# Kernel tuning notes

Measured on AMD Instinct MI355X. Metric: run time of the kernel, lower is better.

## Reference

```python
import jax, jax.numpy as jnp
import numpy as np

NEG_SLOPE = 0.2  # LeakyReLU slope used by standard DGCNN blocks


def _lrelu(v):
    return jnp.where(v >= 0, v, NEG_SLOPE * v)


def _knn_idx(pos, k):
    # pos: [B, N, 3] -> idx: [B, N, k] nearest neighbors by squared distance
    sq = jnp.sum(pos * pos, axis=-1)                       # [B, N]
    d2 = sq[:, :, None] - 2.0 * jnp.einsum('bnc,bmc->bnm', pos, pos) + sq[:, None, :]
    _, idx = jax.lax.top_k(-d2, k)                          # [B, N, k]
    return idx


def _edge_block(x, idx, wa, ba, wb, bb):
    # x: [B, N, C]; idx: [B, N, k]
    nb = jax.vmap(lambda xb, ib: xb[ib])(x, idx)            # [B, N, k, C] gather
    xc = jnp.broadcast_to(x[:, :, None, :], nb.shape)
    feat = jnp.concatenate([xc, nb - xc], axis=-1)          # 'local_global' edge feature [B,N,k,2C]
    h = _lrelu(jnp.einsum('bnkc,cd->bnkd', feat, wa) + ba)
    h = _lrelu(jnp.einsum('bnkc,cd->bnkd', h, wb) + bb)
    return jnp.max(h, axis=2)                               # maxpool over k neighbors -> [B, N, out]


def setup_inputs() -> dict:
    key = jax.random.key(0)
    ks = jax.random.split(key, 24)
    B, N, C = 8, 2048, 3

    def w(k, i, o):
        return jax.random.normal(k, (i, o), jnp.float32) * (1.0 / np.sqrt(i))

    inp = {
        'x': jax.random.normal(ks[0], (B, N, C), jnp.float32),
        'pos': jax.random.normal(ks[1], (B, N, 3), jnp.float32),
        # block1: 2*3 -> 64 -> 64
        'w1a': w(ks[2], 6, 64), 'b1a': jnp.zeros((64,), jnp.float32),
        'w1b': w(ks[3], 64, 64), 'b1b': jnp.zeros((64,), jnp.float32),
        # block2: 2*64 -> 64 -> 128
        'w2a': w(ks[4], 128, 64), 'b2a': jnp.zeros((64,), jnp.float32),
        'w2b': w(ks[5], 64, 128), 'b2b': jnp.zeros((128,), jnp.float32),
        # block3: 2*128 -> 128 -> 512
        'w3a': w(ks[6], 256, 128), 'b3a': jnp.zeros((128,), jnp.float32),
        'w3b': w(ks[7], 128, 512), 'b3b': jnp.zeros((512,), jnp.float32),
        # final head: 704 -> 512 -> 256 -> 12
        'wf1': w(ks[8], 704, 512), 'bf1': jnp.zeros((512,), jnp.float32),
        'wf2': w(ks[9], 512, 256), 'bf2': jnp.zeros((256,), jnp.float32),
        'wf3': w(ks[10], 256, 12), 'bf3': jnp.zeros((12,), jnp.float32),
    }
    return inp


def reference(x, pos, w1a, b1a, w1b, b1b, w2a, b2a, w2b, b2b, w3a, b3a, w3b, b3b,
              wf1, bf1, wf2, bf2, wf3, bf3):
    k = 32
    # kNN graph is built from pos in every block; pos is constant so idx is identical
    idx = _knn_idx(pos, k)
    x1 = _edge_block(x, idx, w1a, b1a, w1b, b1b)            # [B, N, 64]
    x2 = _edge_block(x1, idx, w2a, b2a, w2b, b2b)           # [B, N, 128]
    x3 = _edge_block(x2, idx, w3a, b3a, w3b, b3b)           # [B, N, 512]
    h = jnp.concatenate([x1, x2, x3], axis=2)               # [B, N, 704]
    h = _lrelu(h @ wf1 + bf1)
    h = _lrelu(h @ wf2 + bf2)
    return h @ wf3 + bf3                                    # [B, N, 12]
```

## Files before the change

### kernel.cpp

```cpp
#include <hip/hip_runtime.h>

typedef unsigned short u16;
typedef unsigned int u32;
typedef unsigned long long u64;
typedef short bf16x8 __attribute__((ext_vector_type(8)));
typedef float f32x4 __attribute__((ext_vector_type(4)));
typedef u32 u32x4 __attribute__((ext_vector_type(4)));

__device__ __forceinline__ float b2f(u16 u) {
    return __uint_as_float(((u32)u) << 16);
}
__device__ __forceinline__ u16 f2b(float f) {
    u32 u = __float_as_uint(f);
    u32 r = u + 0x7fffu + ((u >> 16) & 1u);
    return (u16)(r >> 16);
}
__device__ __forceinline__ f32x4 mfma16(bf16x8 a, bf16x8 b, f32x4 c) {
    return __builtin_amdgcn_mfma_f32_16x16x32_bf16(a, b, c, 0, 0, 0);
}

template<int NP, int KP, int R, int C>
__device__ __forceinline__ bool seg(int t, int base, const float* src, u16* dst) {
    int r = t - base;
    if (r < 0) return true;
    constexpr int RNG = NP * KP;
    if (r >= RNG) return false;
    int n = r / KP, k = r - n * KP;
    float v = (k < R && n < C) ? src[k * C + n] : 0.f;
    u16 hi = f2b(v);
    dst[r] = hi;
    dst[RNG + r] = f2b(v - b2f(hi));
    return true;
}
template<int NP, int KP, int R, int C>
__device__ __forceinline__ bool seg_bf(int t, int base, const float* src, u16* dst) {
    int r = t - base;
    if (r < 0) return true;
    constexpr int RNG = NP * KP;
    if (r >= RNG) return false;
    constexpr int KC = KP / 32;
    int j = r & 7, s = r >> 3;
    int lanei = s & 63;
    int ks = (s >> 6) % KC, tile = (s >> 6) / KC;
    int n = tile * 16 + (lanei & 15);
    int k = ks * 32 + (lanei >> 4) * 8 + j;
    float v = (k < R && n < C) ? src[k * C + n] : 0.f;
    u16 hi = f2b(v);
    dst[r] = hi;
    dst[RNG + r] = f2b(v - b2f(hi));
    return true;
}
template<int CMID, int CIN, int KP>
__device__ __forceinline__ bool seg_uv(int t, int base, const float* wa, u16* dst) {
    int r = t - base;
    if (r < 0) return true;
    constexpr int RNG = 2 * CMID * KP;
    if (r >= RNG) return false;
    int n = r / KP, k = r - n * KP;
    float v = 0.f;
    if (k < CIN) {
        if (n < CMID) v = wa[k * CMID + n] - wa[(CIN + k) * CMID + n];
        else          v = wa[(CIN + k) * CMID + (n - CMID)];
    }
    u16 hi = f2b(v);
    dst[r] = hi;
    dst[RNG + r] = f2b(v - b2f(hi));
    return true;
}

__global__ __launch_bounds__(256) void prep_weights(
    const float* w1a, const float* w1b, const float* w2a, const float* w2b,
    const float* w3a, const float* w3b, const float* wf1, const float* wf2,
    const float* wf3,
    u16* t1uv, u16* t2uv, u16* t3uv, u16* t1b, u16* t2b, u16* t3b,
    u16* tf1, u16* tf2, u16* tf3)
{
    int t = blockIdx.x * 256 + threadIdx.x;
    if (seg_uv< 64,   3,  32>(t,      0, w1a, t1uv)) return;
    if (seg_uv< 64,  64,  64>(t,   4096, w2a, t2uv)) return;
    if (seg_uv<128, 128, 128>(t,  12288, w3a, t3uv)) return;
    if (seg_bf< 64,  64,  64,  64>(t,  45056, w1b, t1b)) return;
    if (seg_bf<128,  64,  64, 128>(t,  49152, w2b, t2b)) return;
    if (seg_bf<512, 128, 128, 512>(t,  57344, w3b, t3b)) return;
    if (seg<512, 704, 704, 512>(t, 122880, wf1, tf1)) return;
    if (seg<256, 512, 512, 256>(t, 483328, wf2, tf2)) return;
    if (seg< 16, 256, 256,  12>(t, 614400, wf3, tf3)) return;
}

__device__ __forceinline__ void bitonic256(double v[4], int lane) {
#pragma unroll
    for (int k = 2; k <= 256; k <<= 1) {
#pragma unroll
        for (int j = k >> 1; j > 0; j >>= 1) {
            if (j >= 4) {
                int lj = j >> 2;
                bool upLane = ((lane & (k >> 2)) == 0);
                bool lowLane = ((lane & lj) == 0);
                bool keepMin = (upLane == lowLane);
#pragma unroll
                for (int r = 0; r < 4; ++r) {
                    double o = __shfl_xor(v[r], lj);
                    double mn = fmin(v[r], o), mx = fmax(v[r], o);
                    v[r] = keepMin ? mn : mx;
                }
            } else {
#pragma unroll
                for (int r = 0; r < 4; ++r) {
                    if ((r & j) == 0) {
                        int r2 = r | j;
                        bool up = (((lane * 4 + r) & k) == 0);
                        double mn = fmin(v[r], v[r2]), mx = fmax(v[r], v[r2]);
                        v[r] = up ? mn : mx;
                        v[r2] = up ? mx : mn;
                    }
                }
            }
        }
    }
}

__global__ __launch_bounds__(256) void knn_kernel(const float* __restrict__ pos,
                                                  int* __restrict__ idxout)
{
    int tid = threadIdx.x, lane = tid & 63, wv = tid >> 6;
    int p = blockIdx.x * 4 + wv;
    int b = p >> 11, n = p & 2047;
    __shared__ double cand[4][256];
    const float* pb = pos + (size_t)b * 2048 * 3;
    float pn0 = pb[n * 3 + 0], pn1 = pb[n * 3 + 1], pn2 = pb[n * 3 + 2];
    float sqn = __fadd_rn(__fadd_rn(__fmul_rn(pn0, pn0), __fmul_rn(pn1, pn1)),
                          __fmul_rn(pn2, pn2));
    double kd[32];
#pragma unroll
    for (int j = 0; j < 32; ++j) {
        int m = lane + j * 64;
        float q0 = pb[m * 3 + 0], q1 = pb[m * 3 + 1], q2 = pb[m * 3 + 2];
        float sqm = __fadd_rn(__fadd_rn(__fmul_rn(q0, q0), __fmul_rn(q1, q1)),
                              __fmul_rn(q2, q2));
        float dot = __fadd_rn(__fadd_rn(__fmul_rn(pn0, q0), __fmul_rn(pn1, q1)),
                              __fmul_rn(pn2, q2));
        float d2 = __fadd_rn(__fsub_rn(sqn, __fmul_rn(2.0f, dot)), sqm);
        u32 u = __float_as_uint(d2);
        u = (u & 0x80000000u) ? ~u : (u | 0x80000000u);
        u32 lo = (u << 11) | (u32)m;
        u32 hi = 0x43300000u | (u >> 21);
        kd[j] = __hiloint2double((int)hi, (int)lo);
    }

    double lmin = kd[0];
#pragma unroll
    for (int j = 1; j < 32; ++j) lmin = fmin(lmin, kd[j]);
    double v = lmin;
#pragma unroll
    for (int k = 2; k <= 64; k <<= 1) {
#pragma unroll
        for (int j2 = k >> 1; j2 > 0; j2 >>= 1) {
            double o = __shfl_xor(v, j2);
            bool up = ((lane & k) == 0);
            bool low = ((lane & j2) == 0);
            double mn = fmin(v, o), mx = fmax(v, o);
            v = (up == low) ? mn : mx;
        }
    }
    double T = __shfl(v, 31);

#pragma unroll
    for (int s = 0; s < 4; ++s) cand[wv][lane + s * 64] = 1e300;
    int base = 0;
#pragma unroll
    for (int j = 0; j < 32; ++j) {
        bool pred = (kd[j] <= T);
        u64 bal = __ballot(pred);
        int prefix = (int)__popcll(bal & ((1ull << lane) - 1ull));
        int slot = base + prefix;
        if (pred && slot < 256) cand[wv][slot] = kd[j];
        base += (int)__popcll(bal);
    }

    if (base <= 256) {
        double kc[4];
#pragma unroll
        for (int j = 0; j < 4; ++j) kc[j] = cand[wv][lane * 4 + j];
        bitonic256(kc, lane);
        if (lane < 8) {
            int4 w;
            w.x = __double2loint(kc[0]) & 2047;
            w.y = __double2loint(kc[1]) & 2047;
            w.z = __double2loint(kc[2]) & 2047;
            w.w = __double2loint(kc[3]) & 2047;
            *(int4*)&idxout[(size_t)p * 32 + lane * 4] = w;
        }
    } else {
        double last = -1.0;
        for (int it = 0; it < 32; ++it) {
            double lm0 = 1e300, lm1 = 1e300;
#pragma unroll
            for (int j = 0; j < 32; j += 2) {
                double t0 = kd[j], t1 = kd[j + 1];
                lm0 = fmin(lm0, (t0 > last) ? t0 : 1e300);
                lm1 = fmin(lm1, (t1 > last) ? t1 : 1e300);
            }
            double lm = fmin(lm0, lm1);
#pragma unroll
            for (int off = 32; off; off >>= 1)
                lm = fmin(lm, __shfl_xor(lm, off));
            if (lane == 0) idxout[(size_t)p * 32 + it] = __double2loint(lm) & 2047;
            last = lm;
        }
    }
}

template<int K, int KP, int N2>
__global__ __launch_bounds__(256) void uv_gemm(
    const float* __restrict__ xin, const u16* __restrict__ wT,
    const float* __restrict__ ba, float* __restrict__ Uf, u16* __restrict__ Vb)
{
    constexpr int SA = KP + 8;
    constexpr int WSZ = N2 * KP;
    constexpr int CMID = N2 / 2;
    __shared__ __align__(16) u16 AsH[32 * SA];
    __shared__ __align__(16) u16 AsL[32 * SA];
    int row0 = blockIdx.x * 32;
    int tid = threadIdx.x, lane = tid & 63, wv = tid >> 6, ln = lane & 15, q = lane >> 4;

    for (int e = tid; e < 32 * (KP / 8); e += 256) {
        int r = e / (KP / 8), c0 = (e % (KP / 8)) * 8;
        bf16x8 hv, lv;
#pragma unroll
        for (int jj = 0; jj < 8; ++jj) {
            int c = c0 + jj;
            float v = (c < K) ? xin[(size_t)(row0 + r) * K + c] : 0.f;
            u16 hi = f2b(v);
            hv[jj] = hi;
            lv[jj] = f2b(v - b2f(hi));
        }
        *(bf16x8*)&AsH[r * SA + c0] = hv;
        *(bf16x8*)&AsL[r * SA + c0] = lv;
    }
    __syncthreads();

    constexpr int NT = N2 / 64;
    f32x4 acc[2][NT] = {};
    const int wbase = wv * (N2 / 4);
#pragma unroll
    for (int ks = 0; ks < KP / 32; ++ks) {
        bf16x8 a0h = *(const bf16x8*)&AsH[(ln) * SA + ks * 32 + q * 8];
        bf16x8 a1h = *(const bf16x8*)&AsH[(16 + ln) * SA + ks * 32 + q * 8];
        bf16x8 a0l = *(const bf16x8*)&AsL[(ln) * SA + ks * 32 + q * 8];
        bf16x8 a1l = *(const bf16x8*)&AsL[(16 + ln) * SA + ks * 32 + q * 8];
#pragma unroll
        for (int nt = 0; nt < NT; ++nt) {
            size_t wi = (size_t)(wbase + nt * 16 + ln) * KP + ks * 32 + q * 8;
            bf16x8 bh = *(const bf16x8*)&wT[wi];
            bf16x8 bl = *(const bf16x8*)&wT[WSZ + wi];
            acc[0][nt] = mfma16(a0h, bh, acc[0][nt]);
            acc[0][nt] = mfma16(a0h, bl, acc[0][nt]);
            acc[0][nt] = mfma16(a0l, bh, acc[0][nt]);
            acc[1][nt] = mfma16(a1h, bh, acc[1][nt]);
            acc[1][nt] = mfma16(a1h, bl, acc[1][nt]);
            acc[1][nt] = mfma16(a1l, bh, acc[1][nt]);
        }
    }
#pragma unroll
    for (int nt = 0; nt < NT; ++nt) {
        int col = wbase + nt * 16 + ln;
#pragma unroll
        for (int mt = 0; mt < 2; ++mt)
#pragma unroll
            for (int r = 0; r < 4; ++r) {
                size_t row = (size_t)(row0 + mt * 16 + q * 4 + r);
                if (col < CMID)
                    Uf[row * CMID + col] = acc[mt][nt][r] + ba[col];
                else
                    Vb[row * CMID + (col - CMID)] = f2b(acc[mt][nt][r]);
            }
    }
}

template<int CMID, int COUT, bool OUTB, int PTS, int NTP>
__global__ __launch_bounds__(256, 4) void edge_pool(
    const float* __restrict__ Uf, const u16* __restrict__ Vb,
    const int* __restrict__ idx,
    const u16* __restrict__ wbT, const float* __restrict__ bb,
    void* __restrict__ outp)
{
    constexpr int KC = CMID / 32;
    constexpr int C8 = CMID / 8;
    constexpr int NTW = COUT / 64;
    constexpr int CITER = PTS * 32 * C8 / 256;
    __shared__ __align__(16) u16 hfrag[PTS * 2 * KC * 512];
    __shared__ int nbr[PTS * 32];

    int tid = threadIdx.x, lane = tid & 63, wv = tid >> 6, ln = lane & 15, q = lane >> 4;
    int p0 = blockIdx.x * PTS;

    if (tid < PTS * 32) {
        int pt = tid >> 5, kk = tid & 31;
        int p = p0 + pt;
        nbr[tid] = ((p >> 11) << 11) + (idx[(size_t)p * 32 + kk] & 2047);
    }
    __syncthreads();

#pragma unroll
    for (int e0 = 0; e0 < CITER; ++e0) {
        int e = tid + e0 * 256;
        int pt = e / (32 * C8), rem = e % (32 * C8), r = rem / C8, c8 = rem % C8;
        const float* U = &Uf[(size_t)(p0 + pt) * CMID + c8 * 8];
        bf16x8 vb = *(const bf16x8*)&Vb[(size_t)nbr[pt * 32 + r] * CMID + c8 * 8];
        u32x4 hq;
#pragma unroll
        for (int jj = 0; jj < 4; ++jj) {
            float f0 = U[2 * jj]     + b2f((u16)vb[2 * jj]);
            float f1 = U[2 * jj + 1] + b2f((u16)vb[2 * jj + 1]);
            f0 = f0 >= 0.f ? f0 : 0.2f * f0;
            f1 = f1 >= 0.f ? f1 : 0.2f * f1;
            u32 a = __float_as_uint(f0) + 0x8000u;
            u32 b = __float_as_uint(f1) + 0x8000u;
            hq[jj] = __builtin_amdgcn_perm(b, a, 0x07060302u);
        }
        int mt = r >> 4, lnr = r & 15, ks = c8 >> 2, qq = c8 & 3;
        int slot = qq * 16 + (lnr ^ ((ks << 2) | qq));
        *(u32x4*)&hfrag[(((pt * 2 + mt) * KC + ks) * 64 + slot) * 8] = hq;
    }
    __syncthreads();

    for (int ng = 0; ng < NTW; ng += NTP) {
        f32x4 acc[PTS][2][NTP] = {};
        bf16x8 bh[NTP];
#pragma unroll
        for (int nt = 0; nt < NTP; ++nt) {
            size_t wi = ((size_t)((wv * NTW + ng + nt) * KC + 0) * 64 + lane) * 8;
            bh[nt] = *(const bf16x8*)&wbT[wi];
        }
#pragma unroll
        for (int ks = 0; ks < KC; ++ks) {
            bf16x8 bhn[NTP];
            if (ks + 1 < KC) {
#pragma unroll
                for (int nt = 0; nt < NTP; ++nt) {
                    size_t wi = ((size_t)((wv * NTW + ng + nt) * KC + (ks + 1)) * 64 + lane) * 8;
                    bhn[nt] = *(const bf16x8*)&wbT[wi];
                }
            }
            int slot = q * 16 + (ln ^ ((ks << 2) | q));
#pragma unroll
            for (int pt = 0; pt < PTS; ++pt)
#pragma unroll
                for (int mt = 0; mt < 2; ++mt) {
                    bf16x8 a = *(const bf16x8*)
                        &hfrag[(((pt * 2 + mt) * KC + ks) * 64 + slot) * 8];
#pragma unroll
                    for (int nt = 0; nt < NTP; ++nt)
                        acc[pt][mt][nt] = mfma16(a, bh[nt], acc[pt][mt][nt]);
                }
            if (ks + 1 < KC) {
#pragma unroll
                for (int nt = 0; nt < NTP; ++nt) bh[nt] = bhn[nt];
            }
        }
#pragma unroll
        for (int pt = 0; pt < PTS; ++pt)
#pragma unroll
            for (int nt = 0; nt < NTP; ++nt) {
                int col = wv * (COUT / 4) + (ng + nt) * 16 + ln;
                float m = acc[pt][0][nt][0];
#pragma unroll
                for (int r = 1; r < 4; ++r) m = fmaxf(m, acc[pt][0][nt][r]);
#pragma unroll
                for (int r = 0; r < 4; ++r) m = fmaxf(m, acc[pt][1][nt][r]);
                m = fmaxf(m, __shfl_xor(m, 16));
                m = fmaxf(m, __shfl_xor(m, 32));
                if (q == 0) {
                    float v = m + bb[col];
                    v = v >= 0.f ? v : 0.2f * v;
                    if constexpr (OUTB)
                        ((u16*)outp)[(size_t)(p0 + pt) * COUT + col] = f2b(v);
                    else
                        ((float*)outp)[(size_t)(p0 + pt) * COUT + col] = v;
                }
            }
    }
}

__global__ __launch_bounds__(256) void head1(
    const float* __restrict__ x1, const float* __restrict__ x2,
    const u16* __restrict__ x3,
    const u16* __restrict__ wT, const float* __restrict__ bias,
    u16* __restrict__ out)
{
    constexpr int KD = 704, KT = 352, SA = 360, COUT = 512;
    __shared__ __align__(16) u16 AsH[32 * SA];
    __shared__ __align__(16) u16 AsL[32 * SA];
    int row0 = blockIdx.x * 32;
    int tid = threadIdx.x, lane = tid & 63, wv = tid >> 6, ln = lane & 15, q = lane >> 4;

    f32x4 acc[2][8] = {};
    const int wbase = wv * 128;

    for (int ph = 0; ph < 2; ++ph) {
        if (ph) __syncthreads();
        for (int e = tid; e < 32 * 44; e += 256) {
            int r = e / 44, c8l = e % 44;
            int c = ph * KT + c8l * 8;
            int g = row0 + r;
            int a = r * SA + c8l * 8;
            if (c < 192) {
                const float* src = (c < 64) ? &x1[(size_t)g * 64 + c]
                                            : &x2[(size_t)g * 128 + (c - 64)];
                bf16x8 hv, lv;
#pragma unroll
                for (int jj = 0; jj < 8; ++jj) {
                    float v = src[jj];
                    u16 hi = f2b(v);
                    hv[jj] = hi;
                    lv[jj] = f2b(v - b2f(hi));
                }
                *(bf16x8*)&AsH[a] = hv;
                *(bf16x8*)&AsL[a] = lv;
            } else {
                *(bf16x8*)&AsH[a] = *(const bf16x8*)&x3[(size_t)g * 512 + (c - 192)];
                bf16x8 z = {0, 0, 0, 0, 0, 0, 0, 0};
                *(bf16x8*)&AsL[a] = z;
            }
        }
        __syncthreads();
        for (int ks = 0; ks < 11; ++ks) {
            int gk = ph * 11 + ks;
            bool t3 = (gk < 6);
            bf16x8 a0h = *(const bf16x8*)&AsH[(ln) * SA + ks * 32 + q * 8];
            bf16x8 a1h = *(const bf16x8*)&AsH[(16 + ln) * SA + ks * 32 + q * 8];
            bf16x8 a0l = *(const bf16x8*)&AsL[(ln) * SA + ks * 32 + q * 8];
            bf16x8 a1l = *(const bf16x8*)&AsL[(16 + ln) * SA + ks * 32 + q * 8];
#pragma unroll
            for (int nt = 0; nt < 8; ++nt) {
                size_t wi = (size_t)(wbase + nt * 16 + ln) * KD + gk * 32 + q * 8;
                bf16x8 bh = *(const bf16x8*)&wT[wi];
                acc[0][nt] = mfma16(a0h, bh, acc[0][nt]);
                acc[1][nt] = mfma16(a1h, bh, acc[1][nt]);
                if (t3) {
                    acc[0][nt] = mfma16(a0l, bh, acc[0][nt]);
                    acc[1][nt] = mfma16(a1l, bh, acc[1][nt]);
                }
            }
        }
    }
#pragma unroll
    for (int nt = 0; nt < 8; ++nt) {
        int col = wbase + nt * 16 + ln;
        float bv = bias[col];
#pragma unroll
        for (int mt = 0; mt < 2; ++mt)
#pragma unroll
            for (int r = 0; r < 4; ++r) {
                float v = acc[mt][nt][r] + bv;
                v = v >= 0.f ? v : 0.2f * v;
                out[(size_t)(row0 + mt * 16 + q * 4 + r) * COUT + col] = f2b(v);
            }
    }
}

template<int K, int COUT>
__global__ __launch_bounds__(256) void head_bf(
    const u16* __restrict__ A, const u16* __restrict__ wT,
    const float* __restrict__ bias, u16* __restrict__ out)
{
    constexpr int SA = K + 8;
    __shared__ __align__(16) u16 As[32 * SA];
    int row0 = blockIdx.x * 32;
    int tid = threadIdx.x, lane = tid & 63, wv = tid >> 6, ln = lane & 15, q = lane >> 4;

    for (int e = tid; e < 32 * (K / 8); e += 256) {
        int r = e / (K / 8), c0 = (e % (K / 8)) * 8;
        *(bf16x8*)&As[r * SA + c0] = *(const bf16x8*)&A[(size_t)(row0 + r) * K + c0];
    }
    __syncthreads();

    constexpr int NT = COUT / 64;
    f32x4 acc[2][NT] = {};
    const int wbase = wv * (COUT / 4);
    for (int ks = 0; ks < K / 32; ++ks) {
        bf16x8 a0 = *(const bf16x8*)&As[(ln) * SA + ks * 32 + q * 8];
        bf16x8 a1 = *(const bf16x8*)&As[(16 + ln) * SA + ks * 32 + q * 8];
#pragma unroll
        for (int nt = 0; nt < NT; ++nt) {
            size_t wi = (size_t)(wbase + nt * 16 + ln) * K + ks * 32 + q * 8;
            bf16x8 bh = *(const bf16x8*)&wT[wi];
            acc[0][nt] = mfma16(a0, bh, acc[0][nt]);
            acc[1][nt] = mfma16(a1, bh, acc[1][nt]);
        }
    }
#pragma unroll
    for (int nt = 0; nt < NT; ++nt) {
        int col = wbase + nt * 16 + ln;
        float bv = bias[col];
#pragma unroll
        for (int mt = 0; mt < 2; ++mt)
#pragma unroll
            for (int r = 0; r < 4; ++r) {
                float v = acc[mt][nt][r] + bv;
                v = v >= 0.f ? v : 0.2f * v;
                out[(size_t)(row0 + mt * 16 + q * 4 + r) * COUT + col] = f2b(v);
            }
    }
}

__global__ __launch_bounds__(256) void head_gemm3(
    const u16* __restrict__ A, const u16* __restrict__ wT,
    const float* __restrict__ bias, float* __restrict__ out)
{
    int tid = threadIdx.x, lane = tid & 63, wv = tid >> 6, ln = lane & 15, q = lane >> 4;
    int row0 = (blockIdx.x * 4 + wv) * 32;
    f32x4 acc[2] = {};
#pragma unroll
    for (int ks = 0; ks < 8; ++ks) {
        bf16x8 a0 = *(const bf16x8*)&A[(size_t)(row0 + ln) * 256 + ks * 32 + q * 8];
        bf16x8 a1 = *(const bf16x8*)&A[(size_t)(row0 + 16 + ln) * 256 + ks * 32 + q * 8];
        size_t wi = (size_t)ln * 256 + ks * 32 + q * 8;
        bf16x8 bh = *(const bf16x8*)&wT[wi];
        acc[0] = mfma16(a0, bh, acc[0]);
        acc[1] = mfma16(a1, bh, acc[1]);
    }
    if (ln < 12) {
        float bv = bias[ln];
#pragma unroll
        for (int mt = 0; mt < 2; ++mt)
#pragma unroll
            for (int r = 0; r < 4; ++r)
                out[(size_t)(row0 + mt * 16 + q * 4 + r) * 12 + ln] = acc[mt][r] + bv;
    }
}

extern "C" void kernel_launch(void* const* d_in, const int* in_sizes, int n_in,
                              void* d_out, int out_size, void* d_ws, size_t ws_size,
                              hipStream_t stream)
{
    (void)in_sizes; (void)n_in; (void)out_size; (void)ws_size;
    const float* x   = (const float*)d_in[0];
    const float* pos = (const float*)d_in[1];
    const float* w1a = (const float*)d_in[2];  const float* b1a = (const float*)d_in[3];
    const float* w1b = (const float*)d_in[4];  const float* b1b = (const float*)d_in[5];
    const float* w2a = (const float*)d_in[6];  const float* b2a = (const float*)d_in[7];
    const float* w2b = (const float*)d_in[8];  const float* b2b = (const float*)d_in[9];
    const float* w3a = (const float*)d_in[10]; const float* b3a = (const float*)d_in[11];
    const float* w3b = (const float*)d_in[12]; const float* b3b = (const float*)d_in[13];
    const float* wf1 = (const float*)d_in[14]; const float* bf1 = (const float*)d_in[15];
    const float* wf2 = (const float*)d_in[16]; const float* bf2 = (const float*)d_in[17];
    const float* wf3 = (const float*)d_in[18]; const float* bf3 = (const float*)d_in[19];

    char* ws = (char*)d_ws;
    u16* t1uv = (u16*)(ws + 0);
    u16* t2uv = (u16*)(ws + 16384);
    u16* t3uv = (u16*)(ws + 49152);
    u16* t1b  = (u16*)(ws + 180224);
    u16* t2b  = (u16*)(ws + 196608);
    u16* t3b  = (u16*)(ws + 229376);
    u16* tf1  = (u16*)(ws + 491520);
    u16* tf2  = (u16*)(ws + 1933312);
    u16* tf3  = (u16*)(ws + 2457600);
    int*   idxb = (int*)(ws + 2473984);
    float* x1 = (float*)(ws + 4571136);
    float* x2 = (float*)(ws + 8765440);
    float* Uf = (float*)(ws + 17154048);
    u16*   Vb = (u16*)(ws + 17154048 + 8388608);
    u16*   x3 = (u16*)(ws + 33931264);
    u16*   h1 = (u16*)(ws + 17154048);
    u16*   h2 = (u16*)(ws + 4571136);

    prep_weights<<<2416, 256, 0, stream>>>(w1a, w1b, w2a, w2b, w3a, w3b, wf1, wf2, wf3,
                                           t1uv, t2uv, t3uv, t1b, t2b, t3b, tf1, tf2, tf3);
    knn_kernel<<<4096, 256, 0, stream>>>(pos, idxb);
    uv_gemm<  3, 32, 128><<<512, 256, 0, stream>>>(x,  t1uv, b1a, Uf, Vb);
    edge_pool< 64,  64, false, 2, 1><<<8192, 256, 0, stream>>>(Uf, Vb, idxb, t1b, b1b, x1);
    uv_gemm< 64, 64, 128><<<512, 256, 0, stream>>>(x1, t2uv, b2a, Uf, Vb);
    edge_pool< 64, 128, false, 2, 2><<<8192, 256, 0, stream>>>(Uf, Vb, idxb, t2b, b2b, x2);
    uv_gemm<128, 128, 256><<<512, 256, 0, stream>>>(x2, t3uv, b3a, Uf, Vb);
    edge_pool<128, 512, true, 2, 2><<<8192, 256, 0, stream>>>(Uf, Vb, idxb, t3b, b3b, x3);
    head1<<<512, 256, 0, stream>>>(x1, x2, x3, tf1, bf1, h1);
    head_bf<512, 256><<<512, 256, 0, stream>>>(h1, tf2, bf2, h2);
    head_gemm3<<<128, 256, 0, stream>>>(h2, tf3, bf3, (float*)d_out);
}
```

Measured before the change: 386.0 us.

## Hold edge-pool A fragments in registers and flatten the N-group/K loop

The edge_pool second GEMM now loads all of its A fragments from shared memory into registers once, instead of re-reading them from LDS for every output-column group. The ng and ks loops become a single fully unrolled loop, so the weight prefetch for the next step runs across group boundaries, and the max-pool epilogue fires at the end of each group. This is meant to cut repeated LDS traffic and keep the weight loads pipelined, but it raises VGPR pressure (PTS*2*KC bf16x8 registers held at once). With launch_bounds(256,4) that risks spills or lower occupancy, especially for the CMID=128 block.

Result: no change. 390.0 us (+1.0%).

```diff
diff --git a/kernel.cpp b/kernel.cpp
--- a/kernel.cpp
+++ b/kernel.cpp
@@ -288,6 +288,8 @@
     constexpr int C8 = CMID / 8;
     constexpr int NTW = COUT / 64;
     constexpr int CITER = PTS * 32 * C8 / 256;
+    constexpr int NG = NTW / NTP;
+    constexpr int TT = NG * KC;
     __shared__ __align__(16) u16 hfrag[PTS * 2 * KC * 512];
     __shared__ int nbr[PTS * 32];
 
@@ -324,61 +326,76 @@
     }
     __syncthreads();
 
-    for (int ng = 0; ng < NTW; ng += NTP) {
-        f32x4 acc[PTS][2][NTP] = {};
-        bf16x8 bh[NTP];
-#pragma unroll
-        for (int nt = 0; nt < NTP; ++nt) {
-            size_t wi = ((size_t)((wv * NTW + ng + nt) * KC + 0) * 64 + lane) * 8;
-            bh[nt] = *(const bf16x8*)&wbT[wi];
-        }
+    bf16x8 areg[PTS * 2 * KC];
+#pragma unroll
+    for (int pm = 0; pm < PTS * 2; ++pm)
 #pragma unroll
         for (int ks = 0; ks < KC; ++ks) {
-            bf16x8 bhn[NTP];
-            if (ks + 1 < KC) {
+            int slot = q * 16 + (ln ^ ((ks << 2) | q));
+            areg[pm * KC + ks] = *(const bf16x8*)
+                &hfrag[((pm * KC + ks) * 64 + slot) * 8];
+        }
+
+    f32x4 acc[PTS][2][NTP] = {};
+    bf16x8 bh[NTP];
+#pragma unroll
+    for (int nt = 0; nt < NTP; ++nt) {
+        size_t wi = ((size_t)((wv * NTW + nt) * KC + 0) * 64 + lane) * 8;
+        bh[nt] = *(const bf16x8*)&wbT[wi];
+    }
+#pragma unroll
+    for (int t = 0; t < TT; ++t) {
+        int ks = t % KC, ng = (t / KC) * NTP;
+        bf16x8 bhn[NTP];
+        if (t + 1 < TT) {
+            int ks1 = (t + 1) % KC, ng1 = ((t + 1) / KC) * NTP;
+#pragma unroll
+            for (int nt = 0; nt < NTP; ++nt) {
+                size_t wi = ((size_t)((wv * NTW + ng1 + nt) * KC + ks1) * 64 + lane) * 8;
+                bhn[nt] = *(const bf16x8*)&wbT[wi];
+            }
+        }
+#pragma unroll
+        for (int pt = 0; pt < PTS; ++pt)
+#pragma unroll
+            for (int mt = 0; mt < 2; ++mt) {
+                bf16x8 a = areg[(pt * 2 + mt) * KC + ks];
+#pragma unroll
+                for (int nt = 0; nt < NTP; ++nt)
+                    acc[pt][mt][nt] = mfma16(a, bh[nt], acc[pt][mt][nt]);
+            }
+        if (ks == KC - 1) {
+#pragma unroll
+            for (int pt = 0; pt < PTS; ++pt)
 #pragma unroll
                 for (int nt = 0; nt < NTP; ++nt) {
-                    size_t wi = ((size_t)((wv * NTW + ng + nt) * KC + (ks + 1)) * 64 + lane) * 8;
-                    bhn[nt] = *(const bf16x8*)&wbT[wi];
+                    int col = wv * (COUT / 4) + (ng + nt) * 16 + ln;
+                    float m = acc[pt][0][nt][0];
+#pragma unroll
+                    for (int r = 1; r < 4; ++r) m = fmaxf(m, acc[pt][0][nt][r]);
+#pragma unroll
+                    for (int r = 0; r < 4; ++r) m = fmaxf(m, acc[pt][1][nt][r]);
+                    m = fmaxf(m, __shfl_xor(m, 16));
+                    m = fmaxf(m, __shfl_xor(m, 32));
+                    if (q == 0) {
+                        float v = m + bb[col];
+                        v = v >= 0.f ? v : 0.2f * v;
+                        if constexpr (OUTB)
+                            ((u16*)outp)[(size_t)(p0 + pt) * COUT + col] = f2b(v);
+                        else
+                            ((float*)outp)[(size_t)(p0 + pt) * COUT + col] = v;
+                    }
+#pragma unroll
+                    for (int r = 0; r < 4; ++r) {
+                        acc[pt][0][nt][r] = 0.f;
+                        acc[pt][1][nt][r] = 0.f;
+                    }
                 }
-            }
-            int slot = q * 16 + (ln ^ ((ks << 2) | q));
-#pragma unroll
-            for (int pt = 0; pt < PTS; ++pt)
-#pragma unroll
-                for (int mt = 0; mt < 2; ++mt) {
-                    bf16x8 a = *(const bf16x8*)
-                        &hfrag[(((pt * 2 + mt) * KC + ks) * 64 + slot) * 8];
-#pragma unroll
-                    for (int nt = 0; nt < NTP; ++nt)
-                        acc[pt][mt][nt] = mfma16(a, bh[nt], acc[pt][mt][nt]);
-                }
-            if (ks + 1 < KC) {
-#pragma unroll
-                for (int nt = 0; nt < NTP; ++nt) bh[nt] = bhn[nt];
-            }
-        }
-#pragma unroll
-        for (int pt = 0; pt < PTS; ++pt)
-#pragma unroll
-            for (int nt = 0; nt < NTP; ++nt) {
-                int col = wv * (COUT / 4) + (ng + nt) * 16 + ln;
-                float m = acc[pt][0][nt][0];
-#pragma unroll
-                for (int r = 1; r < 4; ++r) m = fmaxf(m, acc[pt][0][nt][r]);
-#pragma unroll
-                for (int r = 0; r < 4; ++r) m = fmaxf(m, acc[pt][1][nt][r]);
-                m = fmaxf(m, __shfl_xor(m, 16));
-                m = fmaxf(m, __shfl_xor(m, 32));
-                if (q == 0) {
-                    float v = m + bb[col];
-                    v = v >= 0.f ? v : 0.2f * v;
-                    if constexpr (OUTB)
-                        ((u16*)outp)[(size_t)(p0 + pt) * COUT + col] = f2b(v);
-                    else
-                        ((float*)outp)[(size_t)(p0 + pt) * COUT + col] = v;
-                }
-            }
+        }
+        if (t + 1 < TT) {
+#pragma unroll
+            for (int nt = 0; nt < NTP; ++nt) bh[nt] = bhn[nt];
+        }
     }
 }
 
```
